# Kernel optimization log

Measured on AMD Instinct MI355X. Metric: run time of the kernel, lower is better.

The kernel has to match this reference:

```python
import jax, jax.numpy as jnp
import numpy as np

IN_F, OUT_F = 4096, 11008
MAXQ = 15  # 2**4 - 1 for wbits=4


def setup_inputs() -> dict:
    key = jax.random.key(0)
    k1, k2, k3, k4, k5 = jax.random.split(key, 5)
    inp = jax.random.normal(k1, (4, 64, IN_F), dtype=jnp.float32)
    weight = jax.random.normal(k2, (OUT_F, IN_F), dtype=jnp.float32) * 0.02
    bias = jax.random.normal(k3, (OUT_F,), dtype=jnp.float32) * 0.02
    # per-channel asymmetric quant params (as Quantizer.find_params would produce)
    scale = jax.random.uniform(k4, (OUT_F, 1), dtype=jnp.float32) * 0.01 + 1e-4
    zero = jnp.round(jax.random.uniform(k5, (OUT_F, 1), dtype=jnp.float32) * MAXQ)
    return {"input": inp, "weight": weight, "bias": bias,
            "scale": scale, "zero": zero, "maxq": MAXQ}


def reference(input, weight, bias, scale, zero, maxq):
    # fake-quantize weight: q = clamp(round(w/scale) + zero, 0, maxq); w_dq = scale*(q - zero)
    q = jnp.clip(jnp.round(weight / scale) + zero, 0.0, float(maxq))
    w_dq = scale * (q - zero)                      # [out, in]
    # F.linear: input @ w_dq.T + bias
    out = jnp.einsum('bsi,oi->bso', input, w_dq) + bias
    return out
```

## Files before the change

kernel.cpp:

```cpp
#include <hip/hip_runtime.h>
#include <stdint.h>

#define K_TOT 4096
#define N_TOT 11008
#define M_TOT 256
#define BM 128
#define BN 64
#define WST 72

using bf16x8 = __attribute__((ext_vector_type(8))) short;
using f32x4  = __attribute__((ext_vector_type(4))) float;

#define BAR() do {                                          \
    asm volatile("s_waitcnt lgkmcnt(0)" ::: "memory");      \
    __builtin_amdgcn_s_barrier();                           \
    asm volatile("" ::: "memory");                          \
} while (0)

#define MFMA(A, B, C) __builtin_amdgcn_mfma_f32_16x16x32_bf16((A), (B), (C), 0, 0, 0)

__global__ void cvt_a_bf16(const float* __restrict__ in, uint32_t* __restrict__ out) {
    int i = blockIdx.x * blockDim.x + threadIdx.x;
    const float4 v = ((const float4*)in)[i];
    uint32_t a = __float_as_uint(v.x), b = __float_as_uint(v.y),
             c = __float_as_uint(v.z), d = __float_as_uint(v.w);
    a += 0x7FFFu + ((a >> 16) & 1u);
    b += 0x7FFFu + ((b >> 16) & 1u);
    c += 0x7FFFu + ((c >> 16) & 1u);
    d += 0x7FFFu + ((d >> 16) & 1u);
    uint2 o;
    o.x = (a >> 16) | (b & 0xFFFF0000u);
    o.y = (c >> 16) | (d & 0xFFFF0000u);
    ((uint2*)out)[i] = o;
}

__device__ __forceinline__ uint32_t pack_hi16(uint32_t u0, uint32_t u1) {
#if __has_builtin(__builtin_amdgcn_perm)
    return __builtin_amdgcn_perm(u1, u0, 0x07060302u);
#else
    return (u0 >> 16) | (u1 & 0xFFFF0000u);
#endif
}

__device__ __forceinline__ float clamp3(float q, float lo, float hi) {
#if __has_builtin(__builtin_amdgcn_fmed3f)
    return __builtin_amdgcn_fmed3f(q, lo, hi);
#else
    return fminf(fmaxf(q, lo), hi);
#endif
}

__device__ __forceinline__ void dequant16(const f32x4* w, float rs, float lo, float hi,
                                          float sc, uint32_t o[8]) {
    uint32_t u[16];
#pragma unroll
    for (int j = 0; j < 4; ++j) {
#pragma unroll
        for (int e = 0; e < 4; ++e) {
            float q  = rintf(w[j][e] * rs);
            q        = clamp3(q, lo, hi);
            float dq = q * sc;
            uint32_t b = __float_as_uint(dq);
            u[4 * j + e] = b + 0x7FFFu + ((b >> 16) & 1u);
        }
    }
#pragma unroll
    for (int i = 0; i < 8; ++i) o[i] = pack_hi16(u[2 * i], u[2 * i + 1]);
}

#define ITER(STEP, CUR, NXT, P) do {                                            \
    const int _s = (STEP);                                                      \
    const int _koff = _s * 64;                                                  \
              \
    bf16x8 a0 = *(const bf16x8*)(Ap0 + _koff),                                  \
           a1 = *(const bf16x8*)(Ap0 + _koff + 32),                             \
           a2 = *(const bf16x8*)(Ap1 + _koff),                                  \
           a3 = *(const bf16x8*)(Ap1 + _koff + 32),                             \
           a4 = *(const bf16x8*)(Ap2 + _koff),                                  \
           a5 = *(const bf16x8*)(Ap2 + _koff + 32),                             \
           a6 = *(const bf16x8*)(Ap3 + _koff),                                  \
           a7 = *(const bf16x8*)(Ap3 + _koff + 32);                             \
    __builtin_amdgcn_sched_barrier(0);                                          \
     \
    if (_s + 2 < nkt) {                                                         \
        const f32x4* _p = (const f32x4*)(Wp + (size_t)(_s + 2) * 64);           \
        CUR[0] = _p[0]; CUR[1] = _p[1]; CUR[2] = _p[2]; CUR[3] = _p[3];         \
    }                                                                           \
    __builtin_amdgcn_sched_barrier(0);                                          \
                                    \
    {                                                                           \
        bf16x8 b00 = *(const bf16x8*)&sW[P][wn +      (lane & 15)][(lane >> 4) * 8]; \
        bf16x8 b01 = *(const bf16x8*)&sW[P][wn + 16 + (lane & 15)][(lane >> 4) * 8]; \
        acc[0][0] = MFMA(a0, b00, acc[0][0]);                                   \
        acc[0][1] = MFMA(a0, b01, acc[0][1]);                                   \
        acc[1][0] = MFMA(a2, b00, acc[1][0]);                                   \
        acc[1][1] = MFMA(a2, b01, acc[1][1]);                                   \
        acc[2][0] = MFMA(a4, b00, acc[2][0]);                                   \
        acc[2][1] = MFMA(a4, b01, acc[2][1]);                                   \
        acc[3][0] = MFMA(a6, b00, acc[3][0]);                                   \
        acc[3][1] = MFMA(a6, b01, acc[3][1]);                                   \
        bf16x8 b10 = *(const bf16x8*)&sW[P][wn +      (lane & 15)][32 + (lane >> 4) * 8]; \
        bf16x8 b11 = *(const bf16x8*)&sW[P][wn + 16 + (lane & 15)][32 + (lane >> 4) * 8]; \
        acc[0][0] = MFMA(a1, b10, acc[0][0]);                                   \
        acc[0][1] = MFMA(a1, b11, acc[0][1]);                                   \
        acc[1][0] = MFMA(a3, b10, acc[1][0]);                                   \
        acc[1][1] = MFMA(a3, b11, acc[1][1]);                                   \
        acc[2][0] = MFMA(a5, b10, acc[2][0]);                                   \
        acc[2][1] = MFMA(a5, b11, acc[2][1]);                                   \
        acc[3][0] = MFMA(a7, b10, acc[3][0]);                                   \
        acc[3][1] = MFMA(a7, b11, acc[3][1]);                                   \
    }                                                                           \
                     \
    if (_s + 1 < nkt) {                                                         \
        uint32_t o[8];                                                          \
        dequant16(NXT, rs, lo, hi, sc, o);                                      \
        uint16_t* _d = &sW[P ^ 1][nloc][kseg * 16];                             \
        ((uint4*)_d)[0] = make_uint4(o[0], o[1], o[2], o[3]);                   \
        ((uint4*)_d)[1] = make_uint4(o[4], o[5], o[6], o[7]);                   \
    }                                                                           \
    BAR();                                                                      \
} while (0)

__global__ __launch_bounds__(256, 3)
void wql_gemm(const uint16_t* __restrict__ A,
              const float* __restrict__ W,
              const float* __restrict__ scale,
              const float* __restrict__ zero,
              float* __restrict__ P,
              int kloc) {
    __shared__ uint16_t sW[2][BN][WST];

    const int tid  = threadIdx.x;
    const int lane = tid & 63;
    const int wv   = tid >> 6;
    const int wm   = (wv & 1) * 64;
    const int wn   = (wv >> 1) * 32;
    const int m0   = blockIdx.x * BM;
    const int n0   = blockIdx.y * BN;
    const int k0   = blockIdx.z * kloc;
    const int nkt  = kloc >> 6;

    const int nloc = tid >> 2;
    const int kseg = tid & 3;
    const int wrow = n0 + nloc;
    const float* Wp = W + (size_t)wrow * K_TOT + k0 + kseg * 16;
    const float sc = scale[wrow];
    const float zp = zero[wrow];
    const float rs = 1.0f / sc;
    const float lo = -zp, hi = 15.0f - zp;

    const uint16_t* Ap0 = A + (size_t)(m0 + wm +  0 + (lane & 15)) * K_TOT + k0 + (lane >> 4) * 8;
    const uint16_t* Ap1 = A + (size_t)(m0 + wm + 16 + (lane & 15)) * K_TOT + k0 + (lane >> 4) * 8;
    const uint16_t* Ap2 = A + (size_t)(m0 + wm + 32 + (lane & 15)) * K_TOT + k0 + (lane >> 4) * 8;
    const uint16_t* Ap3 = A + (size_t)(m0 + wm + 48 + (lane & 15)) * K_TOT + k0 + (lane >> 4) * 8;

    f32x4 acc[4][2];
#pragma unroll
    for (int mi = 0; mi < 4; ++mi)
#pragma unroll
        for (int ni = 0; ni < 2; ++ni)
            acc[mi][ni] = (f32x4){0.f, 0.f, 0.f, 0.f};

    f32x4 bank0[4], bank1[4];

    {
        const f32x4* p0 = (const f32x4*)Wp;
        bank0[0] = p0[0]; bank0[1] = p0[1]; bank0[2] = p0[2]; bank0[3] = p0[3];
        const f32x4* p1 = (const f32x4*)(Wp + 64);
        bank1[0] = p1[0]; bank1[1] = p1[1]; bank1[2] = p1[2]; bank1[3] = p1[3];
    }
    __builtin_amdgcn_sched_barrier(0);
    {
        uint32_t o[8];
        dequant16(bank0, rs, lo, hi, sc, o);
        uint16_t* d = &sW[0][nloc][kseg * 16];
        ((uint4*)d)[0] = make_uint4(o[0], o[1], o[2], o[3]);
        ((uint4*)d)[1] = make_uint4(o[4], o[5], o[6], o[7]);
    }
    BAR();

    for (int s = 0; s < nkt; s += 2) {
        ITER(s,     bank0, bank1, 0);
        ITER(s + 1, bank1, bank0, 1);
    }

    float* Pb = P + (size_t)blockIdx.z * M_TOT * N_TOT;
    const int colbase = n0 + wn + (lane & 15);
    const int rbase = m0 + wm + ((lane >> 4) << 2);
#pragma unroll
    for (int mi = 0; mi < 4; ++mi) {
#pragma unroll
        for (int ni = 0; ni < 2; ++ni) {
            const int col = colbase + ni * 16;
#pragma unroll
            for (int r = 0; r < 4; ++r) {
                const int row = rbase + mi * 16 + r;
                Pb[(size_t)row * N_TOT + col] = acc[mi][ni][r];
            }
        }
    }
}

__global__ void reduce_bias(const float* __restrict__ P, const float* __restrict__ bias,
                            float* __restrict__ out, int ks) {
    const int i4 = blockIdx.x * blockDim.x + threadIdx.x;
    const size_t tot4 = (size_t)M_TOT * N_TOT / 4;
    const int col = (int)(((size_t)i4 * 4) % N_TOT);
    float4 acc = ((const float4*)P)[i4];
    for (int s = 1; s < ks; ++s) {
        const float4 v = ((const float4*)P)[(size_t)s * tot4 + i4];
        acc.x += v.x; acc.y += v.y; acc.z += v.z; acc.w += v.w;
    }
    const float4 b = *(const float4*)(bias + col);
    acc.x += b.x; acc.y += b.y; acc.z += b.z; acc.w += b.w;
    ((float4*)out)[i4] = acc;
}

extern "C" void kernel_launch(void* const* d_in, const int* in_sizes, int n_in,
                              void* d_out, int out_size, void* d_ws, size_t ws_size,
                              hipStream_t stream) {
    const float* inp    = (const float*)d_in[0];
    const float* weight = (const float*)d_in[1];
    const float* bias   = (const float*)d_in[2];
    const float* scale  = (const float*)d_in[3];
    const float* zero   = (const float*)d_in[4];

    const size_t A_BYTES = (size_t)M_TOT * K_TOT * 2;
    const size_t SLICE   = (size_t)M_TOT * N_TOT * 4;

    uint32_t* Abf = (uint32_t*)d_ws;
    float* partial;
    int KS;
    if (ws_size >= A_BYTES + 4 * SLICE) { KS = 4; partial = (float*)((char*)d_ws + A_BYTES); }
    else if (ws_size >= A_BYTES + 2 * SLICE) { KS = 2; partial = (float*)((char*)d_ws + A_BYTES); }
    else { KS = 1; partial = (float*)d_out; }

    cvt_a_bf16<<<dim3((M_TOT * K_TOT / 4) / 256), dim3(256), 0, stream>>>(inp, Abf);

    dim3 grid(M_TOT / BM, N_TOT / BN, KS);
    wql_gemm<<<grid, dim3(256), 0, stream>>>((const uint16_t*)Abf, weight, scale, zero,
                                             partial, K_TOT / KS);

    reduce_bias<<<dim3((M_TOT * N_TOT / 4) / 256), dim3(256), 0, stream>>>(
        partial, bias, (float*)d_out, KS);
}
```

Measured before the change: 340.4 us.

## Dequantize weights directly into MFMA registers, removing LDS staging and barriers

Replaces the shared-memory weight tile with per-wave register-resident dequantization that feeds MFMA B operands directly, eliminating LDS writes/reads and block barriers. Blocks shrink to two waves over a 128x32 tile, and split-K drops from 4 to 2. bf16 packing uses the hardware packed-convert instruction, and MFMA sections are run at raised priority. Each wave now dequantizes the same weights redundantly and W is fetched twice per block, trading extra ALU and L2 traffic for removed synchronization.

```diff
diff --git a/kernel.cpp b/kernel.cpp
--- a/kernel.cpp
+++ b/kernel.cpp
@@ -4,18 +4,9 @@
 #define K_TOT 4096
 #define N_TOT 11008
 #define M_TOT 256
-#define BM 128
-#define BN 64
-#define WST 72
 
 using bf16x8 = __attribute__((ext_vector_type(8))) short;
 using f32x4  = __attribute__((ext_vector_type(4))) float;
-
-#define BAR() do {                                          \
-    asm volatile("s_waitcnt lgkmcnt(0)" ::: "memory");      \
-    __builtin_amdgcn_s_barrier();                           \
-    asm volatile("" ::: "memory");                          \
-} while (0)
 
 #define MFMA(A, B, C) __builtin_amdgcn_mfma_f32_16x16x32_bf16((A), (B), (C), 0, 0, 0)
 
@@ -34,14 +25,6 @@
     ((uint2*)out)[i] = o;
 }
 
-__device__ __forceinline__ uint32_t pack_hi16(uint32_t u0, uint32_t u1) {
-#if __has_builtin(__builtin_amdgcn_perm)
-    return __builtin_amdgcn_perm(u1, u0, 0x07060302u);
-#else
-    return (u0 >> 16) | (u1 & 0xFFFF0000u);
-#endif
-}
-
 __device__ __forceinline__ float clamp3(float q, float lo, float hi) {
 #if __has_builtin(__builtin_amdgcn_fmed3f)
     return __builtin_amdgcn_fmed3f(q, lo, hi);
@@ -50,109 +33,105 @@
 #endif
 }
 
-__device__ __forceinline__ void dequant16(const f32x4* w, float rs, float lo, float hi,
-                                          float sc, uint32_t o[8]) {
-    uint32_t u[16];
-#pragma unroll
-    for (int j = 0; j < 4; ++j) {
-#pragma unroll
-        for (int e = 0; e < 4; ++e) {
-            float q  = rintf(w[j][e] * rs);
-            q        = clamp3(q, lo, hi);
-            float dq = q * sc;
-            uint32_t b = __float_as_uint(dq);
-            u[4 * j + e] = b + 0x7FFFu + ((b >> 16) & 1u);
-        }
-    }
-#pragma unroll
-    for (int i = 0; i < 8; ++i) o[i] = pack_hi16(u[2 * i], u[2 * i + 1]);
-}
-
-#define ITER(STEP, CUR, NXT, P) do {                                            \
-    const int _s = (STEP);                                                      \
-    const int _koff = _s * 64;                                                  \
-              \
-    bf16x8 a0 = *(const bf16x8*)(Ap0 + _koff),                                  \
-           a1 = *(const bf16x8*)(Ap0 + _koff + 32),                             \
-           a2 = *(const bf16x8*)(Ap1 + _koff),                                  \
-           a3 = *(const bf16x8*)(Ap1 + _koff + 32),                             \
-           a4 = *(const bf16x8*)(Ap2 + _koff),                                  \
-           a5 = *(const bf16x8*)(Ap2 + _koff + 32),                             \
-           a6 = *(const bf16x8*)(Ap3 + _koff),                                  \
-           a7 = *(const bf16x8*)(Ap3 + _koff + 32);                             \
-    __builtin_amdgcn_sched_barrier(0);                                          \
-     \
-    if (_s + 2 < nkt) {                                                         \
-        const f32x4* _p = (const f32x4*)(Wp + (size_t)(_s + 2) * 64);           \
-        CUR[0] = _p[0]; CUR[1] = _p[1]; CUR[2] = _p[2]; CUR[3] = _p[3];         \
-    }                                                                           \
-    __builtin_amdgcn_sched_barrier(0);                                          \
-                                    \
-    {                                                                           \
-        bf16x8 b00 = *(const bf16x8*)&sW[P][wn +      (lane & 15)][(lane >> 4) * 8]; \
-        bf16x8 b01 = *(const bf16x8*)&sW[P][wn + 16 + (lane & 15)][(lane >> 4) * 8]; \
-        acc[0][0] = MFMA(a0, b00, acc[0][0]);                                   \
-        acc[0][1] = MFMA(a0, b01, acc[0][1]);                                   \
-        acc[1][0] = MFMA(a2, b00, acc[1][0]);                                   \
-        acc[1][1] = MFMA(a2, b01, acc[1][1]);                                   \
-        acc[2][0] = MFMA(a4, b00, acc[2][0]);                                   \
-        acc[2][1] = MFMA(a4, b01, acc[2][1]);                                   \
-        acc[3][0] = MFMA(a6, b00, acc[3][0]);                                   \
-        acc[3][1] = MFMA(a6, b01, acc[3][1]);                                   \
-        bf16x8 b10 = *(const bf16x8*)&sW[P][wn +      (lane & 15)][32 + (lane >> 4) * 8]; \
-        bf16x8 b11 = *(const bf16x8*)&sW[P][wn + 16 + (lane & 15)][32 + (lane >> 4) * 8]; \
-        acc[0][0] = MFMA(a1, b10, acc[0][0]);                                   \
-        acc[0][1] = MFMA(a1, b11, acc[0][1]);                                   \
-        acc[1][0] = MFMA(a3, b10, acc[1][0]);                                   \
-        acc[1][1] = MFMA(a3, b11, acc[1][1]);                                   \
-        acc[2][0] = MFMA(a5, b10, acc[2][0]);                                   \
-        acc[2][1] = MFMA(a5, b11, acc[2][1]);                                   \
-        acc[3][0] = MFMA(a7, b10, acc[3][0]);                                   \
-        acc[3][1] = MFMA(a7, b11, acc[3][1]);                                   \
-    }                                                                           \
-                     \
-    if (_s + 1 < nkt) {                                                         \
-        uint32_t o[8];                                                          \
-        dequant16(NXT, rs, lo, hi, sc, o);                                      \
-        uint16_t* _d = &sW[P ^ 1][nloc][kseg * 16];                             \
-        ((uint4*)_d)[0] = make_uint4(o[0], o[1], o[2], o[3]);                   \
-        ((uint4*)_d)[1] = make_uint4(o[4], o[5], o[6], o[7]);                   \
-    }                                                                           \
-    BAR();                                                                      \
+__device__ __forceinline__ bf16x8 deq8(f32x4 x, f32x4 y, float rs, float lo, float hi, float sc) {
+    float d0, d1;
+    union { uint32_t u[4]; bf16x8 v; } o;
+    d0 = clamp3(rintf(x[0] * rs), lo, hi) * sc;
+    d1 = clamp3(rintf(x[1] * rs), lo, hi) * sc;
+    asm("v_cvt_pk_bf16_f32 %0, %1, %2" : "=v"(o.u[0]) : "v"(d0), "v"(d1));
+    d0 = clamp3(rintf(x[2] * rs), lo, hi) * sc;
+    d1 = clamp3(rintf(x[3] * rs), lo, hi) * sc;
+    asm("v_cvt_pk_bf16_f32 %0, %1, %2" : "=v"(o.u[1]) : "v"(d0), "v"(d1));
+    d0 = clamp3(rintf(y[0] * rs), lo, hi) * sc;
+    d1 = clamp3(rintf(y[1] * rs), lo, hi) * sc;
+    asm("v_cvt_pk_bf16_f32 %0, %1, %2" : "=v"(o.u[2]) : "v"(d0), "v"(d1));
+    d0 = clamp3(rintf(y[2] * rs), lo, hi) * sc;
+    d1 = clamp3(rintf(y[3] * rs), lo, hi) * sc;
+    asm("v_cvt_pk_bf16_f32 %0, %1, %2" : "=v"(o.u[3]) : "v"(d0), "v"(d1));
+    return o.v;
+}
+
+#define ITER2(STEP, C, N) do {                                                   \
+    const int _s = (STEP);                                                       \
+    const int _koff = _s * 64;                                                   \
+                  \
+    bf16x8 a0 = *(const bf16x8*)(Ap0 + _koff), a1 = *(const bf16x8*)(Ap0 + _koff + 32), \
+           a2 = *(const bf16x8*)(Ap1 + _koff), a3 = *(const bf16x8*)(Ap1 + _koff + 32), \
+           a4 = *(const bf16x8*)(Ap2 + _koff), a5 = *(const bf16x8*)(Ap2 + _koff + 32), \
+           a6 = *(const bf16x8*)(Ap3 + _koff), a7 = *(const bf16x8*)(Ap3 + _koff + 32); \
+    __builtin_amdgcn_sched_barrier(0);                                           \
+            \
+    if (_s + 1 < nkt) {                                                          \
+        const float* _b0 = Wr0 + _koff + 64;                                     \
+        const float* _b1 = Wr1 + _koff + 64;                                     \
+        w00 = *(const f32x4*)(_b0);      w01 = *(const f32x4*)(_b0 + 4);         \
+        w02 = *(const f32x4*)(_b0 + 32); w03 = *(const f32x4*)(_b0 + 36);        \
+        w10 = *(const f32x4*)(_b1);      w11 = *(const f32x4*)(_b1 + 4);         \
+        w12 = *(const f32x4*)(_b1 + 32); w13 = *(const f32x4*)(_b1 + 36);        \
+    }                                                                            \
+    __builtin_amdgcn_sched_barrier(0);                                           \
+                                \
+    __builtin_amdgcn_s_setprio(1);                                               \
+    acc[0][0] = MFMA(a0, C##00, acc[0][0]);                                      \
+    acc[0][1] = MFMA(a0, C##10, acc[0][1]);                                      \
+    acc[1][0] = MFMA(a2, C##00, acc[1][0]);                                      \
+    acc[1][1] = MFMA(a2, C##10, acc[1][1]);                                      \
+    acc[2][0] = MFMA(a4, C##00, acc[2][0]);                                      \
+    acc[2][1] = MFMA(a4, C##10, acc[2][1]);                                      \
+    acc[3][0] = MFMA(a6, C##00, acc[3][0]);                                      \
+    acc[3][1] = MFMA(a6, C##10, acc[3][1]);                                      \
+    acc[0][0] = MFMA(a1, C##01, acc[0][0]);                                      \
+    acc[0][1] = MFMA(a1, C##11, acc[0][1]);                                      \
+    acc[1][0] = MFMA(a3, C##01, acc[1][0]);                                      \
+    acc[1][1] = MFMA(a3, C##11, acc[1][1]);                                      \
+    acc[2][0] = MFMA(a5, C##01, acc[2][0]);                                      \
+    acc[2][1] = MFMA(a5, C##11, acc[2][1]);                                      \
+    acc[3][0] = MFMA(a7, C##01, acc[3][0]);                                      \
+    acc[3][1] = MFMA(a7, C##11, acc[3][1]);                                      \
+    __builtin_amdgcn_s_setprio(0);                                               \
+    __builtin_amdgcn_sched_barrier(0);                                           \
+      \
+    if (_s + 1 < nkt) {                                                          \
+        N##00 = deq8(w00, w01, rs0, lo0, hi0, sc0);                              \
+        N##01 = deq8(w02, w03, rs0, lo0, hi0, sc0);                              \
+        N##10 = deq8(w10, w11, rs1, lo1, hi1, sc1);                              \
+        N##11 = deq8(w12, w13, rs1, lo1, hi1, sc1);                              \
+    }                                                                            \
 } while (0)
 
-__global__ __launch_bounds__(256, 3)
+__global__ __launch_bounds__(128, 3)
 void wql_gemm(const uint16_t* __restrict__ A,
               const float* __restrict__ W,
               const float* __restrict__ scale,
               const float* __restrict__ zero,
               float* __restrict__ P,
               int kloc) {
-    __shared__ uint16_t sW[2][BN][WST];
-
     const int tid  = threadIdx.x;
     const int lane = tid & 63;
     const int wv   = tid >> 6;
-    const int wm   = (wv & 1) * 64;
-    const int wn   = (wv >> 1) * 32;
-    const int m0   = blockIdx.x * BM;
-    const int n0   = blockIdx.y * BN;
+    const int wm   = wv * 64;
+    const int m0   = blockIdx.x * 128;
+    const int n0   = blockIdx.y * 32;
     const int k0   = blockIdx.z * kloc;
     const int nkt  = kloc >> 6;
 
-    const int nloc = tid >> 2;
-    const int kseg = tid & 3;
-    const int wrow = n0 + nloc;
-    const float* Wp = W + (size_t)wrow * K_TOT + k0 + kseg * 16;
-    const float sc = scale[wrow];
-    const float zp = zero[wrow];
-    const float rs = 1.0f / sc;
-    const float lo = -zp, hi = 15.0f - zp;
-
-    const uint16_t* Ap0 = A + (size_t)(m0 + wm +  0 + (lane & 15)) * K_TOT + k0 + (lane >> 4) * 8;
-    const uint16_t* Ap1 = A + (size_t)(m0 + wm + 16 + (lane & 15)) * K_TOT + k0 + (lane >> 4) * 8;
-    const uint16_t* Ap2 = A + (size_t)(m0 + wm + 32 + (lane & 15)) * K_TOT + k0 + (lane >> 4) * 8;
-    const uint16_t* Ap3 = A + (size_t)(m0 + wm + 48 + (lane & 15)) * K_TOT + k0 + (lane >> 4) * 8;
+    const int l15 = lane & 15;
+    const int lg8 = (lane >> 4) * 8;
+
+    const float sc0 = scale[n0 + l15];
+    const float zp0 = zero[n0 + l15];
+    const float sc1 = scale[n0 + 16 + l15];
+    const float zp1 = zero[n0 + 16 + l15];
+    const float rs0 = 1.0f / sc0, lo0 = -zp0, hi0 = 15.0f - zp0;
+    const float rs1 = 1.0f / sc1, lo1 = -zp1, hi1 = 15.0f - zp1;
+
+    const float* Wr0 = W + (size_t)(n0 + l15) * K_TOT + k0 + lg8;
+    const float* Wr1 = W + (size_t)(n0 + 16 + l15) * K_TOT + k0 + lg8;
+
+    const uint16_t* Ap0 = A + (size_t)(m0 + wm +  0 + l15) * K_TOT + k0 + lg8;
+    const uint16_t* Ap1 = A + (size_t)(m0 + wm + 16 + l15) * K_TOT + k0 + lg8;
+    const uint16_t* Ap2 = A + (size_t)(m0 + wm + 32 + l15) * K_TOT + k0 + lg8;
+    const uint16_t* Ap3 = A + (size_t)(m0 + wm + 48 + l15) * K_TOT + k0 + lg8;
 
     f32x4 acc[4][2];
 #pragma unroll
@@ -161,31 +140,27 @@
         for (int ni = 0; ni < 2; ++ni)
             acc[mi][ni] = (f32x4){0.f, 0.f, 0.f, 0.f};
 
-    f32x4 bank0[4], bank1[4];
+    f32x4 w00, w01, w02, w03, w10, w11, w12, w13;
+    bf16x8 pA00, pA01, pA10, pA11, pB00, pB01, pB10, pB11;
 
     {
-        const f32x4* p0 = (const f32x4*)Wp;
-        bank0[0] = p0[0]; bank0[1] = p0[1]; bank0[2] = p0[2]; bank0[3] = p0[3];
-        const f32x4* p1 = (const f32x4*)(Wp + 64);
-        bank1[0] = p1[0]; bank1[1] = p1[1]; bank1[2] = p1[2]; bank1[3] = p1[3];
-    }
-    __builtin_amdgcn_sched_barrier(0);
-    {
-        uint32_t o[8];
-        dequant16(bank0, rs, lo, hi, sc, o);
-        uint16_t* d = &sW[0][nloc][kseg * 16];
-        ((uint4*)d)[0] = make_uint4(o[0], o[1], o[2], o[3]);
-        ((uint4*)d)[1] = make_uint4(o[4], o[5], o[6], o[7]);
-    }
-    BAR();
+        w00 = *(const f32x4*)(Wr0);      w01 = *(const f32x4*)(Wr0 + 4);
+        w02 = *(const f32x4*)(Wr0 + 32); w03 = *(const f32x4*)(Wr0 + 36);
+        w10 = *(const f32x4*)(Wr1);      w11 = *(const f32x4*)(Wr1 + 4);
+        w12 = *(const f32x4*)(Wr1 + 32); w13 = *(const f32x4*)(Wr1 + 36);
+    }
+    pA00 = deq8(w00, w01, rs0, lo0, hi0, sc0);
+    pA01 = deq8(w02, w03, rs0, lo0, hi0, sc0);
+    pA10 = deq8(w10, w11, rs1, lo1, hi1, sc1);
+    pA11 = deq8(w12, w13, rs1, lo1, hi1, sc1);
 
     for (int s = 0; s < nkt; s += 2) {
-        ITER(s,     bank0, bank1, 0);
-        ITER(s + 1, bank1, bank0, 1);
+        ITER2(s,     pA, pB);
+        ITER2(s + 1, pB, pA);
     }
 
     float* Pb = P + (size_t)blockIdx.z * M_TOT * N_TOT;
-    const int colbase = n0 + wn + (lane & 15);
+    const int colbase = n0 + l15;
     const int rbase = m0 + wm + ((lane >> 4) << 2);
 #pragma unroll
     for (int mi = 0; mi < 4; ++mi) {
@@ -231,14 +206,13 @@
     uint32_t* Abf = (uint32_t*)d_ws;
     float* partial;
     int KS;
-    if (ws_size >= A_BYTES + 4 * SLICE) { KS = 4; partial = (float*)((char*)d_ws + A_BYTES); }
-    else if (ws_size >= A_BYTES + 2 * SLICE) { KS = 2; partial = (float*)((char*)d_ws + A_BYTES); }
+    if (ws_size >= A_BYTES + 2 * SLICE) { KS = 2; partial = (float*)((char*)d_ws + A_BYTES); }
     else { KS = 1; partial = (float*)d_out; }
 
     cvt_a_bf16<<<dim3((M_TOT * K_TOT / 4) / 256), dim3(256), 0, stream>>>(inp, Abf);
 
-    dim3 grid(M_TOT / BM, N_TOT / BN, KS);
-    wql_gemm<<<grid, dim3(256), 0, stream>>>((const uint16_t*)Abf, weight, scale, zero,
+    dim3 grid(M_TOT / 128, N_TOT / 32, KS);
+    wql_gemm<<<grid, dim3(128), 0, stream>>>((const uint16_t*)Abf, weight, scale, zero,
                                              partial, K_TOT / KS);
 
     reduce_bias<<<dim3((M_TOT * N_TOT / 4) / 256), dim3(256), 0, stream>>>(
```

New measurement: 385.8 us. 13.3% more time.
